# Kernel optimization log

Hardware: AMD Instinct MI355X
Metric: run time of the kernel (lower is better)

The kernel has to match this reference:

```python
import jax, jax.numpy as jnp
import numpy as np

N, D = 1024, 512
BS, N_TEXT, N_VIDEO = 64, 16, 16
BETA = 1.0
N_ITERS = 50


def setup_inputs() -> dict:
    key = jax.random.key(0)
    k1, k2 = jax.random.split(key)
    return {
        "t_prob": jax.random.normal(k1, (N, D), dtype=jnp.float32),
        "v_prob": jax.random.normal(k2, (N, D), dtype=jnp.float32),
        "n": N,
        "bs": BS,
        "n_text": N_TEXT,
        "n_video": N_VIDEO,
    }


def _l2norm(x):
    # matches F.normalize(x, p=2, dim=1) (eps irrelevant for randn inputs)
    return x / jnp.linalg.norm(x, axis=1, keepdims=True)


def reference(t_prob, v_prob, n, bs, n_text, n_video):
    dt = t_prob.dtype
    x = _l2norm(t_prob)
    y = _l2norm(v_prob)
    C = 1.0 - x @ y.T                      # [n, n] cosine distance
    A = jnp.exp(-C / BETA)

    sigma0 = jnp.ones((n, 1), dtype=dt) / n
    T0 = jnp.ones((n, n), dtype=dt)

    def step(carry, _):
        T, sigma = carry
        Q = A * T                          # [n, n]
        delta = 1.0 / (n * (Q @ sigma))    # [n, 1]
        sigma_new = 1.0 / (n * (Q.T @ delta))  # [n, 1]
        # diag(delta) @ Q @ diag(sigma) == row/col rescale
        T_new = delta * Q * sigma_new.T
        return (T_new, sigma_new), None

    (T, _), _ = jax.lax.scan(step, (T0, sigma0), None, length=N_ITERS)

    distance_matrix = C.T @ T              # [n, n]
    distance_matrix = distance_matrix.reshape(bs, n_text, bs, n_video).mean(axis=(1, 3))
    dis_loss = jnp.trace(distance_matrix)
    return distance_matrix, dis_loss
```

## Files before the change

kernel.cpp:

```cpp
#include <hip/hip_runtime.h>
#include <math.h>


#define NWG 32
#define TPB 256
#define NIT 50
#define NREP 4

typedef unsigned long long ull;

constexpr int CL_OFF   = 0;
constexpr int CVEC_OFF = 1024 * 1024;
constexpr int CNT_OFF  = CVEC_OFF + 3 * NREP * 1024;

__global__ __launch_bounds__(256) void k_gemm(const float* __restrict__ X,
                                              const float* __restrict__ Y,
                                              float* __restrict__ ws) {
    __shared__ float As[32][68];
    __shared__ float Bs[32][68];
    __shared__ float nX[64], nY[64];
    float* Cl = ws + CL_OFF;

    int tid = threadIdx.x;
    int tx = tid & 15, ty = tid >> 4;
    int bx = blockIdx.x, by = blockIdx.y;
    int lr0 = tid >> 3;
    int kq  = (tid & 7) * 4;

    float acc[4][4] = {};
    float sx0 = 0.f, sx1 = 0.f, sy0 = 0.f, sy1 = 0.f;
    for (int k0 = 0; k0 < 512; k0 += 32) {
        float4 xa = *(const float4*)(X + (size_t)(by * 64 + lr0) * 512 + k0 + kq);
        float4 xb = *(const float4*)(X + (size_t)(by * 64 + lr0 + 32) * 512 + k0 + kq);
        float4 ya = *(const float4*)(Y + (size_t)(bx * 64 + lr0) * 512 + k0 + kq);
        float4 yb = *(const float4*)(Y + (size_t)(bx * 64 + lr0 + 32) * 512 + k0 + kq);
        sx0 += xa.x * xa.x + xa.y * xa.y + xa.z * xa.z + xa.w * xa.w;
        sx1 += xb.x * xb.x + xb.y * xb.y + xb.z * xb.z + xb.w * xb.w;
        sy0 += ya.x * ya.x + ya.y * ya.y + ya.z * ya.z + ya.w * ya.w;
        sy1 += yb.x * yb.x + yb.y * yb.y + yb.z * yb.z + yb.w * yb.w;
        As[kq + 0][lr0] = xa.x; As[kq + 1][lr0] = xa.y;
        As[kq + 2][lr0] = xa.z; As[kq + 3][lr0] = xa.w;
        As[kq + 0][lr0 + 32] = xb.x; As[kq + 1][lr0 + 32] = xb.y;
        As[kq + 2][lr0 + 32] = xb.z; As[kq + 3][lr0 + 32] = xb.w;
        Bs[kq + 0][lr0] = ya.x; Bs[kq + 1][lr0] = ya.y;
        Bs[kq + 2][lr0] = ya.z; Bs[kq + 3][lr0] = ya.w;
        Bs[kq + 0][lr0 + 32] = yb.x; Bs[kq + 1][lr0 + 32] = yb.y;
        Bs[kq + 2][lr0 + 32] = yb.z; Bs[kq + 3][lr0 + 32] = yb.w;
        __syncthreads();
#pragma unroll
        for (int kk = 0; kk < 32; ++kk) {
            float4 a4 = *(const float4*)&As[kk][4 * ty];
            float4 b4 = *(const float4*)&Bs[kk][4 * tx];
            float av[4] = {a4.x, a4.y, a4.z, a4.w};
            float bv[4] = {b4.x, b4.y, b4.z, b4.w};
#pragma unroll
            for (int r = 0; r < 4; ++r)
#pragma unroll
                for (int q = 0; q < 4; ++q) acc[r][q] += av[r] * bv[q];
        }
        __syncthreads();
    }
#pragma unroll
    for (int m = 1; m < 8; m <<= 1) {
        sx0 += __shfl_xor(sx0, m, 64);
        sx1 += __shfl_xor(sx1, m, 64);
        sy0 += __shfl_xor(sy0, m, 64);
        sy1 += __shfl_xor(sy1, m, 64);
    }
    if ((tid & 7) == 0) {
        nX[lr0] = sx0; nX[lr0 + 32] = sx1;
        nY[lr0] = sy0; nY[lr0 + 32] = sy1;
    }
    __syncthreads();

    int i0 = by * 64 + 4 * ty, j0 = bx * 64 + 4 * tx;
    float vy[4];
#pragma unroll
    for (int q = 0; q < 4; ++q) vy[q] = 1.0f / sqrtf(nY[4 * tx + q]);
#pragma unroll
    for (int r = 0; r < 4; ++r) {
        float vx = 1.0f / sqrtf(nX[4 * ty + r]);
        float4 o;
        o.x = acc[r][0] * vx * vy[0] - 1.0f;
        o.y = acc[r][1] * vx * vy[1] - 1.0f;
        o.z = acc[r][2] * vx * vy[2] - 1.0f;
        o.w = acc[r][3] * vx * vy[3] - 1.0f;
        *(float4*)(Cl + (size_t)(i0 + r) * 1024 + j0) = o;
    }
}

__device__ __forceinline__ float f_lo(ull u) { return __uint_as_float((unsigned)u); }
__device__ __forceinline__ float f_hi(ull u) { return __uint_as_float((unsigned)(u >> 32)); }

__global__ __launch_bounds__(256, 1) void k_ipot(float* __restrict__ ws,
                                                 float* __restrict__ out) {
    __shared__ float rws[4][32];
    __shared__ float aLs[32];
    __shared__ float PsRs[4096];
    __shared__ float twv[4];

    const int g = blockIdx.x, tid = threadIdx.x;
    const int rs = tid >> 6, lane = tid & 63;
    const int j0 = rs * 256 + lane * 4;
    float* Cl   = ws + CL_OFF;
    float* cvec = ws + CVEC_OFF;
    unsigned* grp = (unsigned*)(ws + CNT_OFF);

    float E1[32][4], E[32][4], Pp[32];
#pragma unroll
    for (int i = 0; i < 32; ++i) {
        float4 c = *(const float4*)(Cl + (size_t)(g * 32 + i) * 1024 + j0);
        Pp[i] = c.x + c.y + c.z + c.w;
        E1[i][0] = __expf(c.x); E1[i][1] = __expf(c.y);
        E1[i][2] = __expf(c.z); E1[i][3] = __expf(c.w);
        E[i][0] = E1[i][0]; E[i][1] = E1[i][1];
        E[i][2] = E1[i][2]; E[i][3] = E1[i][3];
    }
    float bv[4] = {1.0f, 1.0f, 1.0f, 1.0f};
    float al[32];

    for (int t = 0; t < NIT; ++t) {
        float s0, s1, s2, s3;
        if (t == 0) {
            s0 = s1 = s2 = s3 = 1.0f / 1024.0f;
        } else {
            unsigned tgt = (unsigned)t * 8u;
            long gd = 0;
            while (__hip_atomic_load(&grp[0], __ATOMIC_RELAXED, __HIP_MEMORY_SCOPE_AGENT) < tgt ||
                   __hip_atomic_load(&grp[1], __ATOMIC_RELAXED, __HIP_MEMORY_SCOPE_AGENT) < tgt ||
                   __hip_atomic_load(&grp[2], __ATOMIC_RELAXED, __HIP_MEMORY_SCOPE_AGENT) < tgt ||
                   __hip_atomic_load(&grp[3], __ATOMIC_RELAXED, __HIP_MEMORY_SCOPE_AGENT) < tgt) {
                __builtin_amdgcn_s_sleep(1);
                if (++gd > 3000000) break;
            }
            const ull* rb = (const ull*)(cvec + ((t + 2) % 3) * (NREP * 1024)) + (j0 >> 1);
            ull a0 = __hip_atomic_load(rb + 0,    __ATOMIC_RELAXED, __HIP_MEMORY_SCOPE_AGENT);
            ull a1 = __hip_atomic_load(rb + 1,    __ATOMIC_RELAXED, __HIP_MEMORY_SCOPE_AGENT);
            ull b0 = __hip_atomic_load(rb + 512,  __ATOMIC_RELAXED, __HIP_MEMORY_SCOPE_AGENT);
            ull b1 = __hip_atomic_load(rb + 513,  __ATOMIC_RELAXED, __HIP_MEMORY_SCOPE_AGENT);
            ull c0 = __hip_atomic_load(rb + 1024, __ATOMIC_RELAXED, __HIP_MEMORY_SCOPE_AGENT);
            ull c1 = __hip_atomic_load(rb + 1025, __ATOMIC_RELAXED, __HIP_MEMORY_SCOPE_AGENT);
            ull d0 = __hip_atomic_load(rb + 1536, __ATOMIC_RELAXED, __HIP_MEMORY_SCOPE_AGENT);
            ull d1 = __hip_atomic_load(rb + 1537, __ATOMIC_RELAXED, __HIP_MEMORY_SCOPE_AGENT);
            if (t >= 2 && tid < 64) {
                ull* zb = (ull*)(cvec + ((t + 1) % 3) * (NREP * 1024)) + g * 64 + tid;
                __hip_atomic_store(zb, 0ull, __ATOMIC_RELAXED, __HIP_MEMORY_SCOPE_AGENT);
            }
            float cc0 = f_lo(a0) + f_lo(b0) + f_lo(c0) + f_lo(d0);
            float cc1 = f_hi(a0) + f_hi(b0) + f_hi(c0) + f_hi(d0);
            float cc2 = f_lo(a1) + f_lo(b1) + f_lo(c1) + f_lo(d1);
            float cc3 = f_hi(a1) + f_hi(b1) + f_hi(c1) + f_hi(d1);
            float nb0 = 1.0f / cc0, nb1 = 1.0f / cc1;
            float nb2 = 1.0f / cc2, nb3 = 1.0f / cc3;
            s0 = nb0 * nb0 / bv[0] * (1.0f / 1024.0f); bv[0] = nb0;
            s1 = nb1 * nb1 / bv[1] * (1.0f / 1024.0f); bv[1] = nb1;
            s2 = nb2 * nb2 / bv[2] * (1.0f / 1024.0f); bv[2] = nb2;
            s3 = nb3 * nb3 / bv[3] * (1.0f / 1024.0f); bv[3] = nb3;
        }

        float rp[32];
#pragma unroll
        for (int i = 0; i < 32; ++i)
            rp[i] = E[i][0] * s0 + E[i][1] * s1 + E[i][2] * s2 + E[i][3] * s3;
#pragma unroll
        for (int m = 1; m < 64; m <<= 1)
#pragma unroll
            for (int i = 0; i < 32; ++i) rp[i] += __shfl_xor(rp[i], m, 64);
        if (lane == 0) {
#pragma unroll
            for (int q = 0; q < 8; ++q)
                *(float4*)&rws[rs][4 * q] =
                    make_float4(rp[4*q], rp[4*q+1], rp[4*q+2], rp[4*q+3]);
        }
        __syncthreads();
        if (tid < 32)
            aLs[tid] = 1.0f / (1024.0f * (rws[0][tid] + rws[1][tid] +
                                          rws[2][tid] + rws[3][tid]));
        __syncthreads();
#pragma unroll
        for (int q = 0; q < 8; ++q) {
            float4 a4 = *(const float4*)&aLs[4 * q];
            al[4*q] = a4.x; al[4*q+1] = a4.y; al[4*q+2] = a4.z; al[4*q+3] = a4.w;
        }

        float p0 = 0.f, p1 = 0.f, p2 = 0.f, p3 = 0.f;
#pragma unroll
        for (int i = 0; i < 32; ++i) {
            float ai = al[i];
            p0 += E[i][0] * ai; p1 += E[i][1] * ai;
            p2 += E[i][2] * ai; p3 += E[i][3] * ai;
        }
        float* wb = cvec + (t % 3) * (NREP * 1024) + (g & 3) * 1024 + j0;
        atomicAdd(wb + 0, p0);
        atomicAdd(wb + 1, p1);
        atomicAdd(wb + 2, p2);
        atomicAdd(wb + 3, p3);
        __syncthreads();
        if (tid == 0)
            __hip_atomic_fetch_add(&grp[g >> 3], 1u, __ATOMIC_RELAXED,
                                   __HIP_MEMORY_SCOPE_AGENT);

        if (t < NIT - 1) {
#pragma unroll
            for (int i = 0; i < 32; ++i) {
                E[i][0] *= E1[i][0]; E[i][1] *= E1[i][1];
                E[i][2] *= E1[i][2]; E[i][3] *= E1[i][3];
            }
        }
    }

    {
        unsigned tgt = (unsigned)NIT * 8u;
        long gd = 0;
        while (__hip_atomic_load(&grp[0], __ATOMIC_RELAXED, __HIP_MEMORY_SCOPE_AGENT) < tgt ||
               __hip_atomic_load(&grp[1], __ATOMIC_RELAXED, __HIP_MEMORY_SCOPE_AGENT) < tgt ||
               __hip_atomic_load(&grp[2], __ATOMIC_RELAXED, __HIP_MEMORY_SCOPE_AGENT) < tgt ||
               __hip_atomic_load(&grp[3], __ATOMIC_RELAXED, __HIP_MEMORY_SCOPE_AGENT) < tgt) {
            __builtin_amdgcn_s_sleep(1);
            if (++gd > 3000000) break;
        }
    }
    float bl[4];
    {
        const ull* rb = (const ull*)(cvec + ((NIT - 1) % 3) * (NREP * 1024)) + (j0 >> 1);
        ull a0 = __hip_atomic_load(rb + 0,    __ATOMIC_RELAXED, __HIP_MEMORY_SCOPE_AGENT);
        ull a1 = __hip_atomic_load(rb + 1,    __ATOMIC_RELAXED, __HIP_MEMORY_SCOPE_AGENT);
        ull b0 = __hip_atomic_load(rb + 512,  __ATOMIC_RELAXED, __HIP_MEMORY_SCOPE_AGENT);
        ull b1 = __hip_atomic_load(rb + 513,  __ATOMIC_RELAXED, __HIP_MEMORY_SCOPE_AGENT);
        ull c0 = __hip_atomic_load(rb + 1024, __ATOMIC_RELAXED, __HIP_MEMORY_SCOPE_AGENT);
        ull c1 = __hip_atomic_load(rb + 1025, __ATOMIC_RELAXED, __HIP_MEMORY_SCOPE_AGENT);
        ull d0 = __hip_atomic_load(rb + 1536, __ATOMIC_RELAXED, __HIP_MEMORY_SCOPE_AGENT);
        ull d1 = __hip_atomic_load(rb + 1537, __ATOMIC_RELAXED, __HIP_MEMORY_SCOPE_AGENT);
        bl[0] = 1.0f / (f_lo(a0) + f_lo(b0) + f_lo(c0) + f_lo(d0));
        bl[1] = 1.0f / (f_hi(a0) + f_hi(b0) + f_hi(c0) + f_hi(d0));
        bl[2] = 1.0f / (f_lo(a1) + f_lo(b1) + f_lo(c1) + f_lo(d1));
        bl[3] = 1.0f / (f_hi(a1) + f_hi(b1) + f_hi(c1) + f_hi(d1));
    }

    float* Ps = PsRs;
    float* Rs = PsRs + 2048;
    float Pl[32], Rl[32];
#pragma unroll
    for (int k = 0; k < 32; ++k) {
        Pl[k] = Pp[k];
        Rl[k] = E[k][0] * bl[0] + E[k][1] * bl[1] +
                E[k][2] * bl[2] + E[k][3] * bl[3];
    }
#pragma unroll
    for (int m = 1; m < 4; m <<= 1)
#pragma unroll
        for (int k = 0; k < 32; ++k) {
            Pl[k] += __shfl_xor(Pl[k], m, 64);
            Rl[k] += __shfl_xor(Rl[k], m, 64);
        }
    if ((lane & 3) == 0) {
        int A = rs * 16 + (lane >> 2);
#pragma unroll
        for (int k = 0; k < 32; ++k) {
            Ps[k * 64 + A] = -Pl[k];
            Rs[k * 64 + A] = al[k] * Rl[k];
        }
    }
    __syncthreads();

    float Rk[32];
#pragma unroll
    for (int k = 0; k < 32; ++k) Rk[k] = Rs[k * 64 + lane];
    const float sc = 1.0f / (256.0f * 1024.0f);
    float tsum = 0.0f;
#pragma unroll
    for (int q = 0; q < 16; ++q) {
        int o = tid + 256 * q;
        int A = 4 * q + rs;
        float acc = 0.0f;
#pragma unroll
        for (int k = 0; k < 32; ++k) acc += Ps[k * 64 + A] * Rk[k];
        float val = acc * sc;
        atomicAdd(out + o, val);
        if (A == lane) tsum += val;
    }
#pragma unroll
    for (int m = 1; m < 64; m <<= 1) tsum += __shfl_xor(tsum, m, 64);
    if (lane == 0) twv[rs] = tsum;
    __syncthreads();
    if (tid == 0) atomicAdd(out + 4096, twv[0] + twv[1] + twv[2] + twv[3]);
}

extern "C" void kernel_launch(void* const* d_in, const int* in_sizes, int n_in,
                              void* d_out, int out_size, void* d_ws, size_t ws_size,
                              hipStream_t stream) {
    const float* X = (const float*)d_in[0];
    const float* Y = (const float*)d_in[1];
    float* out = (float*)d_out;
    float* ws  = (float*)d_ws;

    (void)hipMemsetAsync((char*)d_ws + (size_t)CVEC_OFF * 4, 0,
                         (3 * NREP * 1024 + 16) * 4, stream);
    (void)hipMemsetAsync(d_out, 0, (size_t)out_size * 4, stream);

    k_gemm<<<dim3(16, 16), 256, 0, stream>>>(X, Y, ws);
    k_ipot<<<NWG, TPB, 0, stream>>>(ws, out);
}
```

Baseline: 375.4 us.

## Pad barrier counters, poll them in parallel per wave, use transpose-style reduction

The four group arrival counters now sit 128 bytes apart, so they no longer share a cache line, and lanes 0-3 poll them in parallel, combined with a wave vote. The 32-row cross-lane reduction becomes a recursive halving exchange, which cuts shuffle count from 32*6 to about 32. The counter increment moves after the E update, so the state update overlaps the arrival signal. The aim is lower per-iteration barrier latency and fewer shuffle instructions, at the cost of a slightly larger memset.

```diff
diff --git a/kernel.cpp b/kernel.cpp
--- a/kernel.cpp
+++ b/kernel.cpp
@@ -92,6 +92,21 @@
 __device__ __forceinline__ float f_lo(ull u) { return __uint_as_float((unsigned)u); }
 __device__ __forceinline__ float f_hi(ull u) { return __uint_as_float((unsigned)(u >> 32)); }
 
+__device__ __forceinline__ void wavepoll(const unsigned* cnt, int lane,
+                                         unsigned tgt) {
+    int done = (lane < 4)
+        ? (__hip_atomic_load(&cnt[lane * 32], __ATOMIC_RELAXED,
+                             __HIP_MEMORY_SCOPE_AGENT) >= tgt) : 1;
+    long gd = 0;
+    while (!__all(done)) {
+        __builtin_amdgcn_s_sleep(1);
+        if (lane < 4)
+            done = (__hip_atomic_load(&cnt[lane * 32], __ATOMIC_RELAXED,
+                                      __HIP_MEMORY_SCOPE_AGENT) >= tgt);
+        if (++gd > 2000000) break;
+    }
+}
+
 __global__ __launch_bounds__(256, 1) void k_ipot(float* __restrict__ ws,
                                                  float* __restrict__ out) {
     __shared__ float rws[4][32];
@@ -104,7 +119,7 @@
     const int j0 = rs * 256 + lane * 4;
     float* Cl   = ws + CL_OFF;
     float* cvec = ws + CVEC_OFF;
-    unsigned* grp = (unsigned*)(ws + CNT_OFF);
+    unsigned* cnt = (unsigned*)(ws + CNT_OFF);
 
     float E1[32][4], E[32][4], Pp[32];
 #pragma unroll
@@ -124,15 +139,7 @@
         if (t == 0) {
             s0 = s1 = s2 = s3 = 1.0f / 1024.0f;
         } else {
-            unsigned tgt = (unsigned)t * 8u;
-            long gd = 0;
-            while (__hip_atomic_load(&grp[0], __ATOMIC_RELAXED, __HIP_MEMORY_SCOPE_AGENT) < tgt ||
-                   __hip_atomic_load(&grp[1], __ATOMIC_RELAXED, __HIP_MEMORY_SCOPE_AGENT) < tgt ||
-                   __hip_atomic_load(&grp[2], __ATOMIC_RELAXED, __HIP_MEMORY_SCOPE_AGENT) < tgt ||
-                   __hip_atomic_load(&grp[3], __ATOMIC_RELAXED, __HIP_MEMORY_SCOPE_AGENT) < tgt) {
-                __builtin_amdgcn_s_sleep(1);
-                if (++gd > 3000000) break;
-            }
+            wavepoll(cnt, lane, (unsigned)t * 8u);
             const ull* rb = (const ull*)(cvec + ((t + 2) % 3) * (NREP * 1024)) + (j0 >> 1);
             ull a0 = __hip_atomic_load(rb + 0,    __ATOMIC_RELAXED, __HIP_MEMORY_SCOPE_AGENT);
             ull a1 = __hip_atomic_load(rb + 1,    __ATOMIC_RELAXED, __HIP_MEMORY_SCOPE_AGENT);
@@ -158,20 +165,24 @@
             s3 = nb3 * nb3 / bv[3] * (1.0f / 1024.0f); bv[3] = nb3;
         }
 
-        float rp[32];
+        float v[32];
 #pragma unroll
         for (int i = 0; i < 32; ++i)
-            rp[i] = E[i][0] * s0 + E[i][1] * s1 + E[i][2] * s2 + E[i][3] * s3;
-#pragma unroll
-        for (int m = 1; m < 64; m <<= 1)
-#pragma unroll
-            for (int i = 0; i < 32; ++i) rp[i] += __shfl_xor(rp[i], m, 64);
-        if (lane == 0) {
-#pragma unroll
-            for (int q = 0; q < 8; ++q)
-                *(float4*)&rws[rs][4 * q] =
-                    make_float4(rp[4*q], rp[4*q+1], rp[4*q+2], rp[4*q+3]);
-        }
+            v[i] = E[i][0] * s0 + E[i][1] * s1 + E[i][2] * s2 + E[i][3] * s3;
+#pragma unroll
+        for (int st = 0; st < 5; ++st) {
+            const int m = 1 << st;
+            const bool up = (lane & m) != 0;
+#pragma unroll
+            for (int i = 0; i < (16 >> st); ++i) {
+                float x = v[2 * i], y = v[2 * i + 1];
+                float send = up ? x : y;
+                float keep = up ? y : x;
+                v[i] = keep + __shfl_xor(send, m, 64);
+            }
+        }
+        v[0] += __shfl_xor(v[0], 32, 64);
+        if (lane < 32) rws[rs][lane] = v[0];
         __syncthreads();
         if (tid < 32)
             aLs[tid] = 1.0f / (1024.0f * (rws[0][tid] + rws[1][tid] +
@@ -195,10 +206,6 @@
         atomicAdd(wb + 1, p1);
         atomicAdd(wb + 2, p2);
         atomicAdd(wb + 3, p3);
-        __syncthreads();
-        if (tid == 0)
-            __hip_atomic_fetch_add(&grp[g >> 3], 1u, __ATOMIC_RELAXED,
-                                   __HIP_MEMORY_SCOPE_AGENT);
 
         if (t < NIT - 1) {
 #pragma unroll
@@ -207,19 +214,13 @@
                 E[i][2] *= E1[i][2]; E[i][3] *= E1[i][3];
             }
         }
-    }
-
-    {
-        unsigned tgt = (unsigned)NIT * 8u;
-        long gd = 0;
-        while (__hip_atomic_load(&grp[0], __ATOMIC_RELAXED, __HIP_MEMORY_SCOPE_AGENT) < tgt ||
-               __hip_atomic_load(&grp[1], __ATOMIC_RELAXED, __HIP_MEMORY_SCOPE_AGENT) < tgt ||
-               __hip_atomic_load(&grp[2], __ATOMIC_RELAXED, __HIP_MEMORY_SCOPE_AGENT) < tgt ||
-               __hip_atomic_load(&grp[3], __ATOMIC_RELAXED, __HIP_MEMORY_SCOPE_AGENT) < tgt) {
-            __builtin_amdgcn_s_sleep(1);
-            if (++gd > 3000000) break;
-        }
-    }
+        __syncthreads();
+        if (tid == 0)
+            __hip_atomic_fetch_add(&cnt[(g >> 3) * 32], 1u, __ATOMIC_RELAXED,
+                                   __HIP_MEMORY_SCOPE_AGENT);
+    }
+
+    wavepoll(cnt, lane, (unsigned)NIT * 8u);
     float bl[4];
     {
         const ull* rb = (const ull*)(cvec + ((NIT - 1) % 3) * (NREP * 1024)) + (j0 >> 1);
@@ -295,7 +296,7 @@
     float* ws  = (float*)d_ws;
 
     (void)hipMemsetAsync((char*)d_ws + (size_t)CVEC_OFF * 4, 0,
-                         (3 * NREP * 1024 + 16) * 4, stream);
+                         (3 * NREP * 1024 + 128) * 4, stream);
     (void)hipMemsetAsync(d_out, 0, (size_t)out_size * 4, stream);
 
     k_gemm<<<dim3(16, 16), 256, 0, stream>>>(X, Y, ws);
```

New measurement: 346.8 us. 1.08x faster.
